# Kernel optimization log

Hardware: AMD Instinct MI355X
Metric: run time of the kernel (lower is better)

## Reference

```python
import jax, jax.numpy as jnp
import numpy as np

N = 262144   # faces = edges = vertices
E = 2000000  # connections per bipartite edge set
W = 32       # out_width


def _linear_block(x, w, b):
    # LinearBlock(in, out) with defaults -> Linear + LeakyReLU(0.01)
    return jax.nn.leaky_relu(x @ w + b)


def _bip_res_mr_conv(x_src, x_dst, e, w, b):
    # diffs = x_dst[e1] - x_src[e0]; scatter_max over dst; MLP(cat) residual
    diffs = x_dst[e[1]] - x_src[e[0]]                       # [E, W]
    maxes = jax.ops.segment_max(diffs, e[1], num_segments=x_dst.shape[0])
    # torch_scatter.scatter_max fills empty slots with 0
    maxes = jnp.where(jnp.isfinite(maxes), maxes, 0.0)
    h = _linear_block(jnp.concatenate([x_dst, maxes], axis=1), w, b)
    return x_dst + h


def setup_inputs() -> dict:
    key = jax.random.key(0)
    ks = jax.random.split(key, 16)
    inp = {
        "x_f": jax.random.normal(ks[0], (N, 4), dtype=jnp.float32),
        "x_e": jax.random.normal(ks[1], (N, 6), dtype=jnp.float32),
        "x_v": jax.random.normal(ks[2], (N, 3), dtype=jnp.float32),
        "e_fe": jax.random.randint(ks[3], (2, E), 0, N),
        "e_ev": jax.random.randint(ks[4], (2, E), 0, N),
        "e_ef": jax.random.randint(ks[5], (2, E), 0, N),
        "e_ve": jax.random.randint(ks[6], (2, E), 0, N),
    }
    def lin(k, cin, cout):
        s = 1.0 / np.sqrt(cin)
        kw, kb = jax.random.split(k)
        return (jax.random.uniform(kw, (cin, cout), minval=-s, maxval=s, dtype=jnp.float32),
                jax.random.uniform(kb, (cout,), minval=-s, maxval=s, dtype=jnp.float32))
    inp["wf"], inp["bf"] = lin(ks[7], 4, W)
    inp["we"], inp["be"] = lin(ks[8], 6, W)
    inp["wv"], inp["bv"] = lin(ks[9], 3, W)
    inp["w_f2e"], inp["b_f2e"] = lin(ks[10], 2 * W, W)
    inp["w_e2v"], inp["b_e2v"] = lin(ks[11], 2 * W, W)   # E2V conv
    return inp


def reference(x_f, x_e, x_v, e_fe, e_ev, e_ef, e_ve,
              wf, bf, we, be, wv, bv, w_f2e, b_f2e, w_e2v, b_e2v):
    x_f = _linear_block(x_f, wf, bf)
    x_e = _linear_block(x_e, we, be)
    x_v = _linear_block(x_v, wv, bv)
    # NB: original forward reuses self.F2E weights for three convs
    x_e = _bip_res_mr_conv(x_f, x_e, e_fe, w_f2e, b_f2e)
    x_v = _bip_res_mr_conv(x_e, x_v, e_ev, w_e2v, b_e2v)
    x_f = _bip_res_mr_conv(x_e, x_f, e_ef, w_f2e, b_f2e)
    x_e = _bip_res_mr_conv(x_v, x_e, e_ve, w_f2e, b_f2e)
    return (x_f, x_e, x_v)
```

## Files before the change

### kernel.cpp

```cpp
#include <hip/hip_runtime.h>
#include <math.h>

#define N_NODES 262144
#define NE      2000000
#define W_OUT   32

#define NBINS          2048
#define BIN_SHIFT      7
#define NODES_PER_BIN  128
#define CAP            1200
#define MROW           33
#define MXU_DW         (((NODES_PER_BIN + 1) * MROW + 3) & ~3)

__device__ __forceinline__ float lrelu(float x) { return x >= 0.f ? x : 0.01f * x; }

__device__ __forceinline__ unsigned fmin_key(float f) {
    unsigned u = __float_as_uint(f);
    return (u & 0x80000000u) ? ~u : (u | 0x80000000u);
}
__device__ __forceinline__ float fmin_unkey(unsigned u) {
    return __uint_as_float((u & 0x80000000u) ? (u ^ 0x80000000u) : ~u);
}

template<int K>
__global__ void proj_kernel(const float* __restrict__ x, const float* __restrict__ w,
                            const float* __restrict__ b, float* __restrict__ out) {
    __shared__ float wl[K * 32];
    __shared__ float xl[8 * K];
    int t = threadIdx.x;
    for (int i = t; i < K * 32; i += 256) wl[i] = w[i];
    int nbase = blockIdx.x * 8;
    for (int i = t; i < 8 * K; i += 256) xl[i] = x[nbase * K + i];
    __syncthreads();
    int j = t & 31, ln = t >> 5;
    float acc = b[j];
#pragma unroll
    for (int k = 0; k < K; ++k) acc += xl[ln * K + k] * wl[k * 32 + j];
    out[nbase * 32 + t] = lrelu(acc);
}

__global__ __launch_bounds__(512)
void bin_pass3(const int* __restrict__ e0, const int* __restrict__ e1,
               int* __restrict__ gcur, unsigned int* __restrict__ buckets) {
    __shared__ unsigned int hist[NBINS];
    __shared__ unsigned int lcur[NBINS];
    __shared__ unsigned int gbase[NBINS];
    int t = threadIdx.x;
    for (int i = t; i < NBINS; i += 512) hist[i] = 0;
    __syncthreads();

    int q0 = blockIdx.x * 2048 + t;
    int4 d4[4];
#pragma unroll
    for (int k = 0; k < 4; ++k) {
        int q = q0 + k * 512;
        if (q < NE / 4) {
            d4[k] = ((const int4*)e1)[q];
            atomicAdd(&hist[((unsigned)d4[k].x) >> BIN_SHIFT], 1u);
            atomicAdd(&hist[((unsigned)d4[k].y) >> BIN_SHIFT], 1u);
            atomicAdd(&hist[((unsigned)d4[k].z) >> BIN_SHIFT], 1u);
            atomicAdd(&hist[((unsigned)d4[k].w) >> BIN_SHIFT], 1u);
        }
    }
    __syncthreads();
    for (int i = t; i < NBINS; i += 512) {
        gbase[i] = atomicAdd((unsigned int*)&gcur[i], hist[i]);
        lcur[i] = 0;
    }
    __syncthreads();
#pragma unroll
    for (int k = 0; k < 4; ++k) {
        int q = q0 + k * 512;
        if (q < NE / 4) {
            int4 s4 = ((const int4*)e0)[q];
            const int ds[4] = {d4[k].x, d4[k].y, d4[k].z, d4[k].w};
            const int ss[4] = {s4.x, s4.y, s4.z, s4.w};
#pragma unroll
            for (int j = 0; j < 4; ++j) {
                unsigned d = (unsigned)ds[j];
                unsigned bin = d >> BIN_SHIFT;
                unsigned pos = gbase[bin] + atomicAdd(&lcur[bin], 1u);
                if (pos < CAP)
                    buckets[(size_t)bin * CAP + pos] =
                        ((d & (NODES_PER_BIN - 1u)) << 18) | (unsigned)ss[j];
            }
        }
    }
}

__global__ __launch_bounds__(256)
void binreduce6(const int* __restrict__ gcur, const unsigned int* __restrict__ buckets,
                const float* __restrict__ src, const float* __restrict__ dst,
                const float* __restrict__ w, const float* __restrict__ b,
                float* __restrict__ out) {
    __shared__ unsigned int mxu[MXU_DW];
    __shared__ float wl[64 * 32];
    __shared__ __align__(16) float xmat[8][2][64];
    int t = threadIdx.x;
    int bin = blockIdx.x;

    uint4* m4 = (uint4*)mxu;
    for (int i = t; i < MXU_DW / 4; i += 256)
        m4[i] = make_uint4(0xFFFFFFFFu, 0xFFFFFFFFu, 0xFFFFFFFFu, 0xFFFFFFFFu);
    for (int i = t; i < 64 * 32; i += 256) wl[i] = w[i];
    __syncthreads();

    int nb = min(gcur[bin], CAP);
    const unsigned int* bk = buckets + (size_t)bin * CAP;
    const unsigned SENT = (unsigned)NODES_PER_BIN << 18;
    int l = t & 63, wv = t >> 6;
    int g = l >> 3, q = l & 7;
    for (int cb = wv * 64; cb < nb; cb += 256) {
        int idx = cb + l;
        unsigned ent = (idx < nb) ? bk[idx] : SENT;
        float4 v[8];
        unsigned nd[8];
#pragma unroll
        for (int bq = 0; bq < 8; ++bq) {
            unsigned e = __shfl(ent, bq * 8 + g, 64);
            nd[bq] = e >> 18;
            v[bq] = *(const float4*)&src[(size_t)(e & 0x3FFFFu) * 32 + q * 4];
        }
#pragma unroll
        for (int bq = 0; bq < 8; ++bq) {
            unsigned base = nd[bq] * MROW + q * 4;
            atomicMin(&mxu[base + 0], fmin_key(v[bq].x));
            atomicMin(&mxu[base + 1], fmin_key(v[bq].y));
            atomicMin(&mxu[base + 2], fmin_key(v[bq].z));
            atomicMin(&mxu[base + 3], fmin_key(v[bq].w));
        }
    }
    __syncthreads();

    int hw = t >> 5, c = t & 31;
    float bc = b[c];
    size_t gb = (size_t)bin * NODES_PER_BIN;
    for (int grp = 0; grp < 8; ++grp) {
        int n0 = hw * 16 + grp * 2;
#pragma unroll
        for (int gg = 0; gg < 2; ++gg) {
            int node = n0 + gg;
            float dv = dst[(gb + node) * 32 + c];
            unsigned mu = mxu[node * MROW + c];
            float mx = (mu == 0xFFFFFFFFu) ? 0.0f : (dv - fmin_unkey(mu));
            xmat[hw][gg][c] = dv;
            xmat[hw][gg][32 + c] = mx;
        }
        __threadfence_block();

        float acc0 = bc, acc1 = bc;
#pragma unroll 4
        for (int k4 = 0; k4 < 16; ++k4) {
            float w0 = wl[(k4 * 4 + 0) * 32 + c];
            float w1 = wl[(k4 * 4 + 1) * 32 + c];
            float w2 = wl[(k4 * 4 + 2) * 32 + c];
            float w3 = wl[(k4 * 4 + 3) * 32 + c];
            float4 x0 = ((const float4*)xmat[hw][0])[k4];
            float4 x1 = ((const float4*)xmat[hw][1])[k4];
            acc0 += x0.x * w0 + x0.y * w1 + x0.z * w2 + x0.w * w3;
            acc1 += x1.x * w0 + x1.y * w1 + x1.z * w2 + x1.w * w3;
        }
        float dv0 = xmat[hw][0][c];
        float dv1 = xmat[hw][1][c];
        out[(gb + n0 + 0) * 32 + c] = dv0 + lrelu(acc0);
        out[(gb + n0 + 1) * 32 + c] = dv1 + lrelu(acc1);
        __threadfence_block();
    }
}

extern "C" void kernel_launch(void* const* d_in, const int* in_sizes, int n_in,
                              void* d_out, int out_size, void* d_ws, size_t ws_size,
                              hipStream_t stream) {
    const float* x_f  = (const float*)d_in[0];
    const float* x_e  = (const float*)d_in[1];
    const float* x_v  = (const float*)d_in[2];
    const int*   e_fe = (const int*)d_in[3];
    const int*   e_ev = (const int*)d_in[4];
    const int*   e_ef = (const int*)d_in[5];
    const int*   e_ve = (const int*)d_in[6];
    const float* wf    = (const float*)d_in[7];
    const float* bf    = (const float*)d_in[8];
    const float* we    = (const float*)d_in[9];
    const float* be    = (const float*)d_in[10];
    const float* wv    = (const float*)d_in[11];
    const float* bv    = (const float*)d_in[12];
    const float* w_f2e = (const float*)d_in[13];
    const float* b_f2e = (const float*)d_in[14];
    const float* w_e2v = (const float*)d_in[15];
    const float* b_e2v = (const float*)d_in[16];

    float* of = (float*)d_out;
    float* oe = of + (size_t)N_NODES * W_OUT;
    float* ov = oe + (size_t)N_NODES * W_OUT;

    const int NW = N_NODES * W_OUT;

    float*        xe1     = (float*)d_ws;
    unsigned int* buckets = (unsigned int*)(xe1 + NW);
    int*          gcur4   = (int*)(buckets + (size_t)NBINS * CAP);

    dim3 blk(256);
    const int bgrid = (NE / 4 + 2047) / 2048;

    hipMemsetAsync(gcur4, 0, 4 * NBINS * sizeof(int), stream);

    proj_kernel<4><<<N_NODES / 8, blk, 0, stream>>>(x_f, wf, bf, of);
    proj_kernel<6><<<N_NODES / 8, blk, 0, stream>>>(x_e, we, be, oe);
    proj_kernel<3><<<N_NODES / 8, blk, 0, stream>>>(x_v, wv, bv, ov);

    int conv_id = 0;
    auto conv = [&](const float* src, const float* dstb, const int* e,
                    const float* w, const float* bias, float* out) {
        int* gcur = gcur4 + conv_id * NBINS;
        ++conv_id;
        bin_pass3<<<bgrid, dim3(512), 0, stream>>>(e, e + NE, gcur, buckets);
        binreduce6<<<NBINS, blk, 0, stream>>>(gcur, buckets, src, dstb, w, bias, out);
    };

    conv(of,  oe,  e_fe, w_f2e, b_f2e, xe1);
    conv(xe1, ov,  e_ev, w_e2v, b_e2v, ov);
    conv(xe1, of,  e_ef, w_f2e, b_f2e, of);
    conv(ov,  xe1, e_ve, w_f2e, b_f2e, oe);
}
```

Measured before the change: 455.4 us.

## Gather fp16 source copies, halve bin size, and use per-channel lane mapping

The projection and conv kernels now also write a half-precision copy of each node feature array, and the scatter-max gather reads these 2-byte values instead of fp32 to cut gather bandwidth. The gather loop is restructured so 32 lanes handle one edge's 32 channels with scalar loads, replacing the float4 loads spread over 8-lane groups. Bins are halved to 64 nodes (4096 bins, capacity 640) to raise block count and shrink shared-memory state. The fp16 path costs precision in the max-difference term and extra writes. Lower per-bin capacity raises the risk of dropping edges when a bin overflows.

```diff
diff --git a/kernel.cpp b/kernel.cpp
--- a/kernel.cpp
+++ b/kernel.cpp
@@ -1,16 +1,17 @@
 #include <hip/hip_runtime.h>
+#include <hip/hip_fp16.h>
 #include <math.h>
 
 #define N_NODES 262144
 #define NE      2000000
 #define W_OUT   32
 
-#define NBINS          2048
-#define BIN_SHIFT      7
-#define NODES_PER_BIN  128
-#define CAP            1200
+#define NBINS          4096
+#define BIN_SHIFT      6
+#define NODES_PER_BIN  64
+#define CAP            640
 #define MROW           33
-#define MXU_DW         (((NODES_PER_BIN + 1) * MROW + 3) & ~3)
+#define MXU_DW         ((((NODES_PER_BIN + 1) * MROW) + 3) & ~3)
 
 __device__ __forceinline__ float lrelu(float x) { return x >= 0.f ? x : 0.01f * x; }
 
@@ -24,7 +25,8 @@
 
 template<int K>
 __global__ void proj_kernel(const float* __restrict__ x, const float* __restrict__ w,
-                            const float* __restrict__ b, float* __restrict__ out) {
+                            const float* __restrict__ b, float* __restrict__ out,
+                            __half* __restrict__ out_h) {
     __shared__ float wl[K * 32];
     __shared__ float xl[8 * K];
     int t = threadIdx.x;
@@ -36,11 +38,13 @@
     float acc = b[j];
 #pragma unroll
     for (int k = 0; k < K; ++k) acc += xl[ln * K + k] * wl[k * 32 + j];
-    out[nbase * 32 + t] = lrelu(acc);
+    float r = lrelu(acc);
+    out[nbase * 32 + t] = r;
+    if (out_h) out_h[nbase * 32 + t] = __float2half(r);
 }
 
 __global__ __launch_bounds__(512)
-void bin_pass3(const int* __restrict__ e0, const int* __restrict__ e1,
+void bin_pass4(const int* __restrict__ e0, const int* __restrict__ e1,
                int* __restrict__ gcur, unsigned int* __restrict__ buckets) {
     __shared__ unsigned int hist[NBINS];
     __shared__ unsigned int lcur[NBINS];
@@ -64,8 +68,9 @@
     }
     __syncthreads();
     for (int i = t; i < NBINS; i += 512) {
-        gbase[i] = atomicAdd((unsigned int*)&gcur[i], hist[i]);
+        unsigned h = hist[i];
         lcur[i] = 0;
+        if (h) gbase[i] = atomicAdd((unsigned int*)&gcur[i], h);
     }
     __syncthreads();
 #pragma unroll
@@ -88,16 +93,19 @@
     }
 }
 
+template<bool H>
 __global__ __launch_bounds__(256)
-void binreduce6(const int* __restrict__ gcur, const unsigned int* __restrict__ buckets,
-                const float* __restrict__ src, const float* __restrict__ dst,
+void binreduce7(const int* __restrict__ gcur, const unsigned int* __restrict__ buckets,
+                const float* __restrict__ src, const __half* __restrict__ src_h,
+                const float* __restrict__ dst,
                 const float* __restrict__ w, const float* __restrict__ b,
-                float* __restrict__ out) {
+                float* __restrict__ out, __half* __restrict__ out_h) {
     __shared__ unsigned int mxu[MXU_DW];
     __shared__ float wl[64 * 32];
     __shared__ __align__(16) float xmat[8][2][64];
     int t = threadIdx.x;
     int bin = blockIdx.x;
+    int hw = t >> 5, c = t & 31;
 
     uint4* m4 = (uint4*)mxu;
     for (int i = t; i < MXU_DW / 4; i += 256)
@@ -108,35 +116,32 @@
     int nb = min(gcur[bin], CAP);
     const unsigned int* bk = buckets + (size_t)bin * CAP;
     const unsigned SENT = (unsigned)NODES_PER_BIN << 18;
-    int l = t & 63, wv = t >> 6;
-    int g = l >> 3, q = l & 7;
-    for (int cb = wv * 64; cb < nb; cb += 256) {
-        int idx = cb + l;
+    for (int cbase = hw * 32; cbase < nb; cbase += 256) {
+        int idx = cbase + c;
         unsigned ent = (idx < nb) ? bk[idx] : SENT;
-        float4 v[8];
-        unsigned nd[8];
-#pragma unroll
-        for (int bq = 0; bq < 8; ++bq) {
-            unsigned e = __shfl(ent, bq * 8 + g, 64);
-            nd[bq] = e >> 18;
-            v[bq] = *(const float4*)&src[(size_t)(e & 0x3FFFFu) * 32 + q * 4];
-        }
-#pragma unroll
-        for (int bq = 0; bq < 8; ++bq) {
-            unsigned base = nd[bq] * MROW + q * 4;
-            atomicMin(&mxu[base + 0], fmin_key(v[bq].x));
-            atomicMin(&mxu[base + 1], fmin_key(v[bq].y));
-            atomicMin(&mxu[base + 2], fmin_key(v[bq].z));
-            atomicMin(&mxu[base + 3], fmin_key(v[bq].w));
-        }
-    }
-    __syncthreads();
-
-    int hw = t >> 5, c = t & 31;
+#pragma unroll
+        for (int k0 = 0; k0 < 32; k0 += 8) {
+            float v[8];
+            unsigned nd[8];
+#pragma unroll
+            for (int j = 0; j < 8; ++j) {
+                unsigned e = __shfl(ent, k0 + j, 32);
+                nd[j] = e >> 18;
+                size_t off = (size_t)(e & 0x3FFFFu) * 32 + c;
+                if (H) v[j] = __half2float(src_h[off]);
+                else   v[j] = src[off];
+            }
+#pragma unroll
+            for (int j = 0; j < 8; ++j)
+                atomicMin(&mxu[nd[j] * MROW + c], fmin_key(v[j]));
+        }
+    }
+    __syncthreads();
+
     float bc = b[c];
     size_t gb = (size_t)bin * NODES_PER_BIN;
-    for (int grp = 0; grp < 8; ++grp) {
-        int n0 = hw * 16 + grp * 2;
+    for (int grp = 0; grp < 4; ++grp) {
+        int n0 = hw * 8 + grp * 2;
 #pragma unroll
         for (int gg = 0; gg < 2; ++gg) {
             int node = n0 + gg;
@@ -160,10 +165,14 @@
             acc0 += x0.x * w0 + x0.y * w1 + x0.z * w2 + x0.w * w3;
             acc1 += x1.x * w0 + x1.y * w1 + x1.z * w2 + x1.w * w3;
         }
-        float dv0 = xmat[hw][0][c];
-        float dv1 = xmat[hw][1][c];
-        out[(gb + n0 + 0) * 32 + c] = dv0 + lrelu(acc0);
-        out[(gb + n0 + 1) * 32 + c] = dv1 + lrelu(acc1);
+        float r0 = xmat[hw][0][c] + lrelu(acc0);
+        float r1 = xmat[hw][1][c] + lrelu(acc1);
+        out[(gb + n0 + 0) * 32 + c] = r0;
+        out[(gb + n0 + 1) * 32 + c] = r1;
+        if (out_h) {
+            out_h[(gb + n0 + 0) * 32 + c] = __float2half(r0);
+            out_h[(gb + n0 + 1) * 32 + c] = __float2half(r1);
+        }
         __threadfence_block();
     }
 }
@@ -193,32 +202,44 @@
     float* oe = of + (size_t)N_NODES * W_OUT;
     float* ov = oe + (size_t)N_NODES * W_OUT;
 
-    const int NW = N_NODES * W_OUT;
+    const size_t NW = (size_t)N_NODES * W_OUT;
 
     float*        xe1     = (float*)d_ws;
     unsigned int* buckets = (unsigned int*)(xe1 + NW);
     int*          gcur4   = (int*)(buckets + (size_t)NBINS * CAP);
+    __half*       SA      = (__half*)(gcur4 + 4 * NBINS);
+    __half*       SB      = SA + NW;
+
+    const size_t need = NW * 4 + (size_t)NBINS * CAP * 4 + 4 * NBINS * 4 + 2 * NW * 2;
+    const bool useH = ws_size >= need;
+    if (!useH) { SA = nullptr; SB = nullptr; }
 
     dim3 blk(256);
     const int bgrid = (NE / 4 + 2047) / 2048;
 
     hipMemsetAsync(gcur4, 0, 4 * NBINS * sizeof(int), stream);
 
-    proj_kernel<4><<<N_NODES / 8, blk, 0, stream>>>(x_f, wf, bf, of);
-    proj_kernel<6><<<N_NODES / 8, blk, 0, stream>>>(x_e, we, be, oe);
-    proj_kernel<3><<<N_NODES / 8, blk, 0, stream>>>(x_v, wv, bv, ov);
+    proj_kernel<4><<<N_NODES / 8, blk, 0, stream>>>(x_f, wf, bf, of, SA);
+    proj_kernel<6><<<N_NODES / 8, blk, 0, stream>>>(x_e, we, be, oe, nullptr);
+    proj_kernel<3><<<N_NODES / 8, blk, 0, stream>>>(x_v, wv, bv, ov, nullptr);
 
     int conv_id = 0;
-    auto conv = [&](const float* src, const float* dstb, const int* e,
-                    const float* w, const float* bias, float* out) {
+    auto conv = [&](const float* src, const __half* src_h, const float* dstb,
+                    const int* e, const float* w, const float* bias,
+                    float* out, __half* out_h) {
         int* gcur = gcur4 + conv_id * NBINS;
         ++conv_id;
-        bin_pass3<<<bgrid, dim3(512), 0, stream>>>(e, e + NE, gcur, buckets);
-        binreduce6<<<NBINS, blk, 0, stream>>>(gcur, buckets, src, dstb, w, bias, out);
+        bin_pass4<<<bgrid, dim3(512), 0, stream>>>(e, e + NE, gcur, buckets);
+        if (src_h)
+            binreduce7<true><<<NBINS, blk, 0, stream>>>(gcur, buckets, src, src_h,
+                                                        dstb, w, bias, out, out_h);
+        else
+            binreduce7<false><<<NBINS, blk, 0, stream>>>(gcur, buckets, src, nullptr,
+                                                         dstb, w, bias, out, out_h);
     };
 
-    conv(of,  oe,  e_fe, w_f2e, b_f2e, xe1);
-    conv(xe1, ov,  e_ev, w_e2v, b_e2v, ov);
-    conv(xe1, of,  e_ef, w_f2e, b_f2e, of);
-    conv(ov,  xe1, e_ve, w_f2e, b_f2e, oe);
-}
+    conv(of,  SA, oe, e_fe, w_f2e, b_f2e, xe1, SB);
+    conv(xe1, SB, ov, e_ev, w_e2v, b_e2v, ov,  SA);
+    conv(xe1, SB, of, e_ef, w_f2e, b_f2e, of,  nullptr);
+    conv(ov,  SA, xe1, e_ve, w_f2e, b_f2e, oe, nullptr);
+}
```

Measured after the change: 481.5 us. 1.06x slower.
